# Optimization experiments

Hardware: AMD Instinct MI355X
Metric: run time of the kernel (lower is better)

Reference implementation:

```python
import jax, jax.numpy as jnp
import numpy as np

B, N, IN_F = 4, 2048, 256
H, HEAD_DIM = 8, 32  # out_features=256, concat=True -> head_dim=32
ALPHA = 0.2
MASK_VAL = -9e15


def setup_inputs() -> dict:
    key = jax.random.key(0)
    k1, k2, k3, k4 = jax.random.split(key, 4)
    x = jax.random.normal(k1, (B, N, IN_F), dtype=jnp.float32)
    adj = jax.random.randint(k2, (B, N, N), 0, 2, dtype=jnp.int32)
    # xavier_uniform for W [H, in, head_dim]: gain=1, fan_in=in, fan_out=head_dim
    limW = float(np.sqrt(6.0 / (IN_F + HEAD_DIM)))
    W = jax.random.uniform(k3, (H, IN_F, HEAD_DIM), dtype=jnp.float32, minval=-limW, maxval=limW)
    # xavier_uniform for a [H, 2*head_dim]: fan_in=2*head_dim, fan_out=H (2D tensor)
    lima = float(np.sqrt(6.0 / (H + 2 * HEAD_DIM)))
    a = jax.random.uniform(k4, (H, 2 * HEAD_DIM), dtype=jnp.float32, minval=-lima, maxval=lima)
    return {"x": x, "adj": adj, "W": W, "a": a}


def reference(x, adj, W, a):
    # x: [B, N, F], adj: [B, N, N], W: [H, F, D], a: [H, 2D]
    D = W.shape[-1]
    Wh = jnp.einsum('bnf,hfd->bhnd', x, W)                     # [B,H,N,D]
    a_src, a_dst = a[:, :D], a[:, D:]
    # additive score e_ij = a_src . Wh_i + a_dst . Wh_j (equivalent to concat+matmul)
    e_i = jnp.einsum('bhnd,hd->bhn', Wh, a_src)                # [B,H,N]
    e_j = jnp.einsum('bhnd,hd->bhn', Wh, a_dst)                # [B,H,N]
    scores = e_i[:, :, :, None] + e_j[:, :, None, :]           # [B,H,N,N]
    scores = jnp.where(scores > 0, scores, ALPHA * scores)     # LeakyReLU
    scores = jnp.where(adj[:, None, :, :] == 0, MASK_VAL, scores)
    probs = jax.nn.softmax(scores, axis=-1)                    # [B,H,N,N]
    h = jnp.einsum('bhij,bhjd->bhid', probs, Wh)               # [B,H,N,D]
    b, n = x.shape[0], x.shape[1]
    return h.transpose(0, 2, 1, 3).reshape(b, n, h.shape[1] * D)  # concat heads
```

## Files before the change

kernel.cpp:

```cpp
#include <hip/hip_runtime.h>

#define BB 4
#define NN 2048
#define INF 256
#define HH 8
#define DD 32
#define LOG2E 1.4426950408889634f

typedef __attribute__((ext_vector_type(8))) _Float16 half8;
typedef __attribute__((ext_vector_type(2))) _Float16 h2;
typedef __attribute__((ext_vector_type(4))) float f32x4;
typedef __attribute__((address_space(3))) unsigned as3_u32;
typedef __attribute__((address_space(1))) const unsigned as1_u32;

__device__ __forceinline__ unsigned short f16u(float v) {
    union { _Float16 f; unsigned short u; } c;
    c.f = (_Float16)v;
    return c.u;
}

__global__ __launch_bounds__(256) void adjprep_kernel(
    const int* __restrict__ adj, const float* __restrict__ W,
    const float* __restrict__ a, unsigned* __restrict__ bitsG,
    float* __restrict__ we_g)
{
    const int bid = blockIdx.x, t = threadIdx.x;
    if (bid < 2048) {
        const int wv = t >> 6, l = t & 63;
        const int row = bid * 4 + wv;
        const int* ap = adj + (size_t)row * NN;
        int vreg[32];
        #pragma unroll
        for (int c = 0; c < 32; ++c) vreg[c] = ap[c * 64 + l];
        unsigned myw = 0;
        #pragma unroll
        for (int c = 0; c < 32; ++c) {
            unsigned long long m = __ballot(vreg[c] != 0);
            unsigned sel = (l & 1) ? (unsigned)(m >> 32) : (unsigned)m;
            myw = ((l >> 1) == c) ? sel : myw;
        }
        bitsG[(size_t)row * 64 + l] = myw;
        return;
    }
    const int k = bid - 2048;
    const int h = k & 7, sel = k >> 3;
    const float* wr = W + ((size_t)(h * INF + t)) * DD;
    const float* av = a + h * 2 * DD + sel * DD;
    float acc = 0.f;
    #pragma unroll
    for (int d = 0; d < DD; ++d) acc += wr[d] * av[d];
    we_g[k * INF + t] = acc * LOG2E;
}

__global__ __launch_bounds__(256) void prepw_kernel(
    const float* __restrict__ x, const float* __restrict__ W,
    const float* __restrict__ we_g, unsigned short* __restrict__ whT2,
    float* __restrict__ esrc, unsigned* __restrict__ ejE,
    unsigned* __restrict__ ejF)
{
    __shared__ __align__(16) unsigned short smem[64 * 264 * 2];
    const int bid = blockIdx.x, t = threadIdx.x;
    const int role = bid & 1, id = bid >> 1;

    if (role == 0) {
        unsigned short* xb = smem;
        unsigned short* wb = smem + 64 * 264;
        const int hp = id & 3, tl = (id >> 2) & 31, b = id >> 7;
        const int n0 = tl * 64;

        #pragma unroll
        for (int p = 0; p < 16; ++p) {
            int flat = p * 1024 + t * 4;
            int row = flat >> 8, col = flat & 255;
            f32x4 g = *(const f32x4*)&x[((size_t)(b * NN + n0 + row)) * INF + col];
            union { h2 h; unsigned u; } c0, c1;
            c0.h = (h2){(_Float16)g[0], (_Float16)g[1]};
            c1.h = (h2){(_Float16)g[2], (_Float16)g[3]};
            uint2 pk; pk.x = c0.u; pk.y = c1.u;
            *(uint2*)&xb[row * 264 + col] = pk;
        }
        #pragma unroll
        for (int p = 0; p < 16; ++p) {
            int flat = p * 1024 + t * 4;
            int h2i = flat >> 13, rem = flat & 8191;
            int f = rem >> 5, d0 = rem & 31;
            f32x4 g = *(const f32x4*)&W[(((size_t)(hp * 2 + h2i)) * INF + f) * DD + d0];
            #pragma unroll
            for (int i = 0; i < 4; ++i)
                wb[(h2i * 32 + d0 + i) * 264 + f] = f16u(g[i]);
        }
        __syncthreads();

        const int w = t >> 6, l = t & 63;
        const int ml = l & 15, q = l >> 4;
        f32x4 acc[4] = {};
        const unsigned short* apx = &xb[(w * 16 + ml) * 264 + q * 8];
        #pragma unroll
        for (int k0 = 0; k0 < INF; k0 += 32) {
            half8 A = *(const half8*)&apx[k0];
            #pragma unroll
            for (int c16 = 0; c16 < 4; ++c16) {
                half8 Bf = *(const half8*)&wb[(c16 * 16 + ml) * 264 + q * 8 + k0];
                acc[c16] = __builtin_amdgcn_mfma_f32_16x16x32_f16(A, Bf, acc[c16], 0, 0, 0);
            }
        }
        __syncthreads();
        unsigned short* ldsC = xb;
        #pragma unroll
        for (int c16 = 0; c16 < 4; ++c16)
            #pragma unroll
            for (int r = 0; r < 4; ++r) {
                int col = c16 * 16 + ml;
                int rt  = w * 16 + q * 4 + r;
                ldsC[col * 72 + rt] = f16u(acc[c16][r]);
            }
        __syncthreads();
        #pragma unroll
        for (int p = 0; p < 2; ++p) {
            int g = p * 256 + t;
            int d = g & 31, jo = (g >> 5) & 7, hh = g >> 8;
            half8 vv = *(const half8*)&ldsC[(hh * 32 + d) * 72 + jo * 8];
            int bh = b * 8 + hp * 2 + hh;
            *(half8*)&whT2[(((size_t)bh * 256 + tl * 8 + jo) * 32 + d) * 8] = vv;
        }
        return;
    }

    float* xs    = (float*)smem;
    float* weld2 = (float*)smem + 16 * 260;
    const int tile = id & 127, b = id >> 7;
    const int n0 = tile * 16;

    #pragma unroll
    for (int p = 0; p < 4; ++p) {
        int flat = p * 1024 + t * 4;
        int row = flat >> 8, col = flat & 255;
        f32x4 g = *(const f32x4*)&x[((size_t)(b * NN + n0 + row)) * INF + col];
        *(f32x4*)&xs[row * 260 + col] = g;
    }
    #pragma unroll
    for (int p = 0; p < 4; ++p) {
        int flat = p * 1024 + t * 4;
        int k = flat >> 8, f = flat & 255;
        f32x4 g = *(const f32x4*)&we_g[flat];
        *(f32x4*)&weld2[(f >> 4) * 260 + k * 16 + (f & 15)] = g;
    }
    __syncthreads();

    const int row = t >> 4, cc = t & 15;
    f32x4 xv[4];
    #pragma unroll
    for (int i = 0; i < 4; ++i)
        xv[i] = *(const f32x4*)&xs[row * 260 + cc * 16 + i * 4];

    float keep = 0.f;
    #pragma unroll
    for (int k = 0; k < 16; ++k) {
        float s = 0.f;
        #pragma unroll
        for (int i = 0; i < 4; ++i) {
            f32x4 w4 = *(const f32x4*)&weld2[cc * 260 + k * 16 + i * 4];
            s += xv[i][0]*w4[0] + xv[i][1]*w4[1] + xv[i][2]*w4[2] + xv[i][3]*w4[3];
        }
        s += __shfl_xor(s, 1, 64);
        s += __shfl_xor(s, 2, 64);
        s += __shfl_xor(s, 4, 64);
        s += __shfl_xor(s, 8, 64);
        keep = (cc == k) ? s : keep;
    }
    const int n = n0 + row;
    float Ej = __builtin_amdgcn_exp2f(keep);
    float Fj = __builtin_amdgcn_exp2f(0.2f * keep);
    unsigned eh = (unsigned)f16u(Ej);
    unsigned fh = (unsigned)f16u(Fj);
    unsigned eo = (unsigned)__shfl_xor((int)eh, 16, 64);
    unsigned fo = (unsigned)__shfl_xor((int)fh, 16, 64);
    if (cc < 8) {
        esrc[(b * 8 + cc) * NN + n] = keep;
    } else if (!(row & 1)) {
        int bh = b * 8 + (cc - 8);
        ejE[bh * 1024 + n / 2] = (eo << 16) | eh;
        ejF[bh * 1024 + n / 2] = (fo << 16) | fh;
    }
}

__global__ __launch_bounds__(512, 8) void attn_kernel(
    const unsigned short* __restrict__ whT2, const float* __restrict__ esrc,
    const unsigned* __restrict__ ejE, const unsigned* __restrict__ ejF,
    const unsigned* __restrict__ bitsG, float* __restrict__ out)
{
    __shared__ __align__(16) unsigned short whs[2][2][4096];
    __shared__ __align__(16) unsigned epsE[2][2][64];
    __shared__ __align__(16) unsigned epsF[2][2][64];
    const int t = threadIdx.x, w = t >> 6, l = t & 63;
    const int rw = w & 3, js = w >> 2;
    const int ml = l & 15, q = l >> 4;
    const int obid = blockIdx.x;
    const int bid = (obid & 7) * 128 + (obid >> 3);
    const int ig = bid & 31, h = (bid >> 5) & 7, b = bid >> 8;
    const int bh = b * HH + h;
    const int i0 = ig * 64 + rw * 16;

    const float ei = esrc[bh * NN + i0 + ml];
    const float Gi = __builtin_amdgcn_exp2f(-0.8f * ei);
    const h2 gi2 = {(_Float16)Gi, (_Float16)Gi};

    const unsigned short* whb = whT2 + (size_t)bh * (256 * 256);
    const unsigned* epE = ejE + bh * 1024;
    const unsigned* epF = ejF + bh * 1024;
    const unsigned* mbase = bitsG + ((size_t)(b * NN + i0 + ml)) * 64 + js * 32;

    auto stage = [&](int it, int buf) {
        const char* g = (const char*)whb + (js * 8 + it) * 8192 + rw * 2048 + l * 16;
        unsigned short* ld = &whs[buf][js][rw * 1024];
        __builtin_amdgcn_global_load_lds((as1_u32*)g, (as3_u32*)ld, 16, 0, 0);
        __builtin_amdgcn_global_load_lds((as1_u32*)(g + 1024), (as3_u32*)(ld + 512), 16, 0, 0);
        if (rw == 0) {
            __builtin_amdgcn_global_load_lds((as1_u32*)(epE + (js * 8 + it) * 64 + l),
                                             (as3_u32*)&epsE[buf][js][0], 4, 0, 0);
            __builtin_amdgcn_global_load_lds((as1_u32*)(epF + (js * 8 + it) * 64 + l),
                                             (as3_u32*)&epsF[buf][js][0], 4, 0, 0);
        }
    };

    const half8 hones = {(_Float16)1.f, (_Float16)1.f, (_Float16)1.f, (_Float16)1.f,
                         (_Float16)1.f, (_Float16)1.f, (_Float16)1.f, (_Float16)1.f};
    f32x4 accP = {}, accQ = {}, accD = {};

    stage(0, 0);
    uint4 mrow = *(const uint4*)&mbase[0];
    for (int it = 0; it < 8; ++it) {
        __syncthreads();
        if (it < 7) stage(it + 1, (it + 1) & 1);
        const int buf = it & 1;
        const uint4 mcur = mrow;
        if (it < 7) mrow = *(const uint4*)&mbase[(it + 1) * 4];
        const unsigned mw[4] = {mcur.x, mcur.y, mcur.z, mcur.w};
        #pragma unroll
        for (int k = 0; k < 4; ++k) {
            const unsigned short* wp = &whs[buf][js][(k * 4 + q) * 256];
            half8 B0 = *(const half8*)&wp[ml * 8];
            half8 B1 = *(const half8*)&wp[(16 + ml) * 8];
            uint4 eA = *(const uint4*)&epsE[buf][js][k * 16 + q * 4];
            uint4 fA = *(const uint4*)&epsF[buf][js][k * 16 + q * 4];
            unsigned st = mw[k] >> (q * 8);
            union { unsigned u[4]; half8 s; } f0;
            const unsigned* ea = &eA.x;
            const unsigned* fa = &fA.x;
            #pragma unroll
            for (int pp = 0; pp < 4; ++pp) {
                union { unsigned u; h2 h; } uE, uF, uP;
                uE.u = ea[pp]; uF.u = fa[pp];
                uP.h = __builtin_elementwise_max(uF.h * gi2, uE.h);
                unsigned mA = (unsigned)__builtin_amdgcn_sbfe(st, 2 * pp, 1);
                unsigned mB = (unsigned)__builtin_amdgcn_sbfe(st, 2 * pp + 1, 1);
                unsigned m32 = __builtin_amdgcn_perm(mB, mA, 0x05040100u);
                f0.u[pp] = uP.u & m32;
            }
            accP = __builtin_amdgcn_mfma_f32_16x16x32_f16(f0.s, B0, accP, 0, 0, 0);
            accQ = __builtin_amdgcn_mfma_f32_16x16x32_f16(f0.s, B1, accQ, 0, 0, 0);
            accD = __builtin_amdgcn_mfma_f32_16x16x32_f16(f0.s, hones, accD, 0, 0, 0);
        }
    }

    __syncthreads();
    float* cmb = (float*)&whs[0][0][0];
    float* myc = &cmb[(rw * 64 + l) * 13];
    if (js == 1) {
        *(f32x4*)&myc[0] = accP;
        *(f32x4*)&myc[4] = accQ;
        *(f32x4*)&myc[8] = accD;
    }
    __syncthreads();
    if (js == 0) {
        f32x4 oP = *(const f32x4*)&myc[0];
        f32x4 oQ = *(const f32x4*)&myc[4];
        f32x4 oD = *(const f32x4*)&myc[8];
        #pragma unroll
        for (int r = 0; r < 4; ++r) {
            int ir = i0 + q * 4 + r;
            float inv = 1.0f / (accD[r] + oD[r]);
            size_t ba = ((size_t)(b * NN + ir)) * (HH * DD) + h * DD;
            out[ba + ml]      = (accP[r] + oP[r]) * inv;
            out[ba + 16 + ml] = (accQ[r] + oQ[r]) * inv;
        }
    }
}

extern "C" void kernel_launch(void* const* d_in, const int* in_sizes, int n_in,
                              void* d_out, int out_size, void* d_ws, size_t ws_size,
                              hipStream_t stream) {
    (void)in_sizes; (void)n_in; (void)out_size; (void)ws_size;
    const float* x   = (const float*)d_in[0];
    const int*   adj = (const int*)d_in[1];
    const float* W   = (const float*)d_in[2];
    const float* a   = (const float*)d_in[3];
    float* out = (float*)d_out;

    char* ws = (char*)d_ws;
    unsigned short* whT2 = (unsigned short*)ws;
    float*    esrc  = (float*)(ws + (4u << 20));
    unsigned* ejE   = (unsigned*)(ws + (4u << 20) + (256u << 10));
    unsigned* ejF   = (unsigned*)(ws + (4u << 20) + (384u << 10));
    unsigned* bitsG = (unsigned*)(ws + (4u << 20) + (512u << 10));
    float*    we_g  = (float*)(ws + (4u << 20) + (512u << 10) + (2u << 20));

    adjprep_kernel<<<dim3(2064), dim3(256), 0, stream>>>(adj, W, a, bitsG, we_g);
    prepw_kernel  <<<dim3(1024), dim3(256), 0, stream>>>(x, W, we_g, whT2, esrc, ejE, ejF);
    attn_kernel   <<<dim3(1024), dim3(512), 0, stream>>>(whT2, esrc, ejE, ejF, bitsG, out);
}
```

Before: 142.2 us.

## Pre-transpose W to f16 once and load MFMA operands directly from global

The adjprep kernel now also writes a transposed f16 copy of W, using 16 extra blocks. Each prepw role-0 block then reads its MFMA A and B fragments straight from global memory instead of staging x and W through padded LDS tiles. The role-1 path likewise reads x rows directly. This cuts LDS use, so more blocks fit per CU (launch bounds set to 4), and removes a sync and a repeated per-block transpose of W, at the cost of uncoalesced or redundant global and cache loads.

```diff
diff --git a/kernel.cpp b/kernel.cpp
--- a/kernel.cpp
+++ b/kernel.cpp
@@ -22,7 +22,7 @@
 __global__ __launch_bounds__(256) void adjprep_kernel(
     const int* __restrict__ adj, const float* __restrict__ W,
     const float* __restrict__ a, unsigned* __restrict__ bitsG,
-    float* __restrict__ we_g)
+    float* __restrict__ we_g, unsigned short* __restrict__ wTf16)
 {
     const int bid = blockIdx.x, t = threadIdx.x;
     if (bid < 2048) {
@@ -43,69 +43,61 @@
         return;
     }
     const int k = bid - 2048;
-    const int h = k & 7, sel = k >> 3;
-    const float* wr = W + ((size_t)(h * INF + t)) * DD;
-    const float* av = a + h * 2 * DD + sel * DD;
-    float acc = 0.f;
-    #pragma unroll
-    for (int d = 0; d < DD; ++d) acc += wr[d] * av[d];
-    we_g[k * INF + t] = acc * LOG2E;
-}
-
-__global__ __launch_bounds__(256) void prepw_kernel(
-    const float* __restrict__ x, const float* __restrict__ W,
+    if (k < 16) {
+        const int h = k & 7, sel = k >> 3;
+        const float* wr = W + ((size_t)(h * INF + t)) * DD;
+        const float* av = a + h * 2 * DD + sel * DD;
+        float acc = 0.f;
+        #pragma unroll
+        for (int d = 0; d < DD; ++d) acc += wr[d] * av[d];
+        we_g[k * INF + t] = acc * LOG2E;
+    }
+    #pragma unroll
+    for (int r2 = 0; r2 < 8; ++r2) {
+        int row = k * 8 + r2;
+        int h = row >> 5, d = row & 31;
+        wTf16[row * INF + t] = f16u(W[((size_t)(h * INF + t)) * DD + d]);
+    }
+}
+
+__global__ __launch_bounds__(256, 4) void prepw_kernel(
+    const float* __restrict__ x, const unsigned short* __restrict__ wTf16,
     const float* __restrict__ we_g, unsigned short* __restrict__ whT2,
     float* __restrict__ esrc, unsigned* __restrict__ ejE,
     unsigned* __restrict__ ejF)
 {
-    __shared__ __align__(16) unsigned short smem[64 * 264 * 2];
+    __shared__ __align__(16) float smem[16 * 260];
     const int bid = blockIdx.x, t = threadIdx.x;
     const int role = bid & 1, id = bid >> 1;
 
     if (role == 0) {
-        unsigned short* xb = smem;
-        unsigned short* wb = smem + 64 * 264;
+        unsigned short* ldsC = (unsigned short*)smem;
         const int hp = id & 3, tl = (id >> 2) & 31, b = id >> 7;
         const int n0 = tl * 64;
-
-        #pragma unroll
-        for (int p = 0; p < 16; ++p) {
-            int flat = p * 1024 + t * 4;
-            int row = flat >> 8, col = flat & 255;
-            f32x4 g = *(const f32x4*)&x[((size_t)(b * NN + n0 + row)) * INF + col];
-            union { h2 h; unsigned u; } c0, c1;
-            c0.h = (h2){(_Float16)g[0], (_Float16)g[1]};
-            c1.h = (h2){(_Float16)g[2], (_Float16)g[3]};
-            uint2 pk; pk.x = c0.u; pk.y = c1.u;
-            *(uint2*)&xb[row * 264 + col] = pk;
-        }
-        #pragma unroll
-        for (int p = 0; p < 16; ++p) {
-            int flat = p * 1024 + t * 4;
-            int h2i = flat >> 13, rem = flat & 8191;
-            int f = rem >> 5, d0 = rem & 31;
-            f32x4 g = *(const f32x4*)&W[(((size_t)(hp * 2 + h2i)) * INF + f) * DD + d0];
-            #pragma unroll
-            for (int i = 0; i < 4; ++i)
-                wb[(h2i * 32 + d0 + i) * 264 + f] = f16u(g[i]);
-        }
-        __syncthreads();
-
         const int w = t >> 6, l = t & 63;
         const int ml = l & 15, q = l >> 4;
+
+        const float* xrow = &x[((size_t)(b * NN + n0 + w * 16 + ml)) * INF + q * 8];
+        half8 A[8];
+        #pragma unroll
+        for (int k0 = 0; k0 < 8; ++k0) {
+            f32x4 g0 = *(const f32x4*)&xrow[k0 * 32];
+            f32x4 g1 = *(const f32x4*)&xrow[k0 * 32 + 4];
+            A[k0] = (half8){(_Float16)g0[0], (_Float16)g0[1],
+                            (_Float16)g0[2], (_Float16)g0[3],
+                            (_Float16)g1[0], (_Float16)g1[1],
+                            (_Float16)g1[2], (_Float16)g1[3]};
+        }
         f32x4 acc[4] = {};
-        const unsigned short* apx = &xb[(w * 16 + ml) * 264 + q * 8];
-        #pragma unroll
-        for (int k0 = 0; k0 < INF; k0 += 32) {
-            half8 A = *(const half8*)&apx[k0];
+        #pragma unroll
+        for (int k0 = 0; k0 < 8; ++k0) {
             #pragma unroll
             for (int c16 = 0; c16 < 4; ++c16) {
-                half8 Bf = *(const half8*)&wb[(c16 * 16 + ml) * 264 + q * 8 + k0];
-                acc[c16] = __builtin_amdgcn_mfma_f32_16x16x32_f16(A, Bf, acc[c16], 0, 0, 0);
+                half8 Bf = *(const half8*)
+                    &wTf16[(size_t)(hp * 64 + c16 * 16 + ml) * INF + q * 8 + k0 * 32];
+                acc[c16] = __builtin_amdgcn_mfma_f32_16x16x32_f16(A[k0], Bf, acc[c16], 0, 0, 0);
             }
         }
-        __syncthreads();
-        unsigned short* ldsC = xb;
         #pragma unroll
         for (int c16 = 0; c16 < 4; ++c16)
             #pragma unroll
@@ -126,18 +118,10 @@
         return;
     }
 
-    float* xs    = (float*)smem;
-    float* weld2 = (float*)smem + 16 * 260;
+    float* weld2 = smem;
     const int tile = id & 127, b = id >> 7;
     const int n0 = tile * 16;
 
-    #pragma unroll
-    for (int p = 0; p < 4; ++p) {
-        int flat = p * 1024 + t * 4;
-        int row = flat >> 8, col = flat & 255;
-        f32x4 g = *(const f32x4*)&x[((size_t)(b * NN + n0 + row)) * INF + col];
-        *(f32x4*)&xs[row * 260 + col] = g;
-    }
     #pragma unroll
     for (int p = 0; p < 4; ++p) {
         int flat = p * 1024 + t * 4;
@@ -148,10 +132,10 @@
     __syncthreads();
 
     const int row = t >> 4, cc = t & 15;
+    const float* xr = &x[((size_t)(b * NN + n0 + row)) * INF + cc * 16];
     f32x4 xv[4];
     #pragma unroll
-    for (int i = 0; i < 4; ++i)
-        xv[i] = *(const f32x4*)&xs[row * 260 + cc * 16 + i * 4];
+    for (int i = 0; i < 4; ++i) xv[i] = *(const f32x4*)&xr[i * 4];
 
     float keep = 0.f;
     #pragma unroll
@@ -304,8 +288,10 @@
     unsigned* ejF   = (unsigned*)(ws + (4u << 20) + (384u << 10));
     unsigned* bitsG = (unsigned*)(ws + (4u << 20) + (512u << 10));
     float*    we_g  = (float*)(ws + (4u << 20) + (512u << 10) + (2u << 20));
-
-    adjprep_kernel<<<dim3(2064), dim3(256), 0, stream>>>(adj, W, a, bitsG, we_g);
-    prepw_kernel  <<<dim3(1024), dim3(256), 0, stream>>>(x, W, we_g, whT2, esrc, ejE, ejF);
+    unsigned short* wTf16 = (unsigned short*)(ws + (4u << 20) + (512u << 10)
+                                              + (2u << 20) + (16u << 10));
+
+    adjprep_kernel<<<dim3(2080), dim3(256), 0, stream>>>(adj, W, a, bitsG, we_g, wTf16);
+    prepw_kernel  <<<dim3(1024), dim3(256), 0, stream>>>(x, wTf16, we_g, whT2, esrc, ejE, ejF);
     attn_kernel   <<<dim3(1024), dim3(512), 0, stream>>>(whT2, esrc, ejE, ejF, bitsG, out);
 }
```

New measurement: 151.5 us. +6.6%, slower.
